# Kernel optimization log

Hardware: AMD Instinct MI355X
Metric: run time of the kernel (lower is better)

The kernel has to match this reference:

```python
import jax, jax.numpy as jnp
import numpy as np

E, T, H, I = 32, 512, 2048, 768


def setup_inputs() -> dict:
    key = jax.random.key(0)
    k1, k2, k3, k4 = jax.random.split(key, 4)
    scale = 1.0 / np.sqrt(H)
    return {
        "routed_input": jax.random.normal(k1, (E, T, H), dtype=jnp.float32),
        "gate_proj": jax.random.normal(k2, (E, I, H), dtype=jnp.float32) * scale,
        "up_proj": jax.random.normal(k3, (E, I, H), dtype=jnp.float32) * scale,
        "down_proj": jax.random.normal(k4, (E, H, I), dtype=jnp.float32) * scale,
    }


def reference(routed_input, gate_proj, up_proj, down_proj):
    # routed_input: [E, T, H]; per-expert SwiGLU MLP, concat over experts.
    gate = jnp.einsum("eth,eih->eti", routed_input, gate_proj)
    up = jnp.einsum("eth,eih->eti", routed_input, up_proj)
    hidden = jax.nn.silu(gate) * up  # [E, T, I]
    out = jnp.einsum("eti,ehi->eth", hidden, down_proj)  # [E, T, H]
    return out.reshape(E * T, H)
```

## Files before the change

kernel.cpp:

```cpp
#include <hip/hip_runtime.h>


#define NE 32
#define NT 512
#define NH 2048
#define NI 768

typedef short        short8  __attribute__((ext_vector_type(8)));
typedef float        floatx4 __attribute__((ext_vector_type(4)));
typedef unsigned int uintx4  __attribute__((ext_vector_type(4)));
typedef __attribute__((address_space(1))) const unsigned int g_u32;
typedef __attribute__((address_space(3))) unsigned int l_u32;

__device__ __forceinline__ void gl_lds16(const void* g, void* l) {
    __builtin_amdgcn_global_load_lds((g_u32*)g, (l_u32*)l, 16, 0, 0);
}

__device__ __forceinline__ unsigned int cvt_pk_bf16(float lo, float hi) {
    unsigned int r;
    asm("v_cvt_pk_bf16_f32 %0, %1, %2" : "=v"(r) : "v"(lo), "v"(hi));
    return r;
}

__device__ __forceinline__ short8 frag8(floatx4 x0, floatx4 x1) {
    union { unsigned int u[4]; short8 s; } t;
    t.u[0] = cvt_pk_bf16(x0[0], x0[1]);
    t.u[1] = cvt_pk_bf16(x0[2], x0[3]);
    t.u[2] = cvt_pk_bf16(x1[0], x1[1]);
    t.u[3] = cvt_pk_bf16(x1[2], x1[3]);
    return t.s;
}

__device__ __forceinline__ uintx4 pack8(floatx4 x0, floatx4 x1) {
    uintx4 u;
    u[0] = cvt_pk_bf16(x0[0], x0[1]);
    u[1] = cvt_pk_bf16(x0[2], x0[3]);
    u[2] = cvt_pk_bf16(x1[0], x1[1]);
    u[3] = cvt_pk_bf16(x1[2], x1[3]);
    return u;
}

__device__ __forceinline__ ushort f2bf(float f) {
    union { float f; unsigned int u; } v; v.f = f;
    unsigned int r = v.u + 0x7fffu + ((v.u >> 16) & 1u);
    return (ushort)(r >> 16);
}

__global__ __launch_bounds__(512, 1) void moe_gateup(
    const float* __restrict__ rin, const float* __restrict__ gate,
    const float* __restrict__ up, ushort* __restrict__ hidden)
{
    __shared__ ushort S[2][3][128][32];

    const int bid = blockIdx.x;
    const int wg  = (bid & 7) * 96 + (bid >> 3);
    const int e   = wg / 24;
    const int rem = wg % 24;
    const int ti  = rem % 6;
    const int tm  = rem / 6;

    const int tid  = threadIdx.x;
    const int lane = tid & 63;
    const int wave = tid >> 6;
    const int wr = wave >> 2;
    const int wc = wave & 3;

    const float* Ab = rin  + (size_t)e * NT * NH + (size_t)(tm * 128) * NH;
    const float* Gb = gate + (size_t)e * NI * NH + (size_t)(ti * 128) * NH;
    const float* Ub = up   + (size_t)e * NI * NH + (size_t)(ti * 128) * NH;

    const int s_row = wave * 16 + (lane >> 2);
    const int s_cl  = lane & 3;
    const int s_c   = s_cl ^ (s_row & 3);
    const float* As_src = Ab + (size_t)s_row * NH + s_c * 8;
    const float* Gs_src = Gb + (size_t)s_row * NH + s_c * 8;
    const float* Us_src = Ub + (size_t)s_row * NH + s_c * 8;

    floatx4 accg[4][2], accu[4][2];
    #pragma unroll
    for (int m = 0; m < 4; ++m)
        #pragma unroll
        for (int n = 0; n < 2; ++n) {
            accg[m][n] = (floatx4)0.f;
            accu[m][n] = (floatx4)0.f;
        }

    const int frow = lane & 15;
    const int h    = lane >> 4;
    const int KT = NH / 32;

    floatx4 pA0[3][2], pA1[3][2];

#define ISSUE(kt, P) do {                                                    \
        const int k_ = (kt) * 32;                                            \
        P[0][0] = *(const floatx4*)(As_src + k_);                            \
        P[0][1] = *(const floatx4*)(As_src + k_ + 4);                        \
        P[1][0] = *(const floatx4*)(Gs_src + k_);                            \
        P[1][1] = *(const floatx4*)(Gs_src + k_ + 4);                        \
        P[2][0] = *(const floatx4*)(Us_src + k_);                            \
        P[2][1] = *(const floatx4*)(Us_src + k_ + 4);                        \
    } while (0)

#define WRITE(b, P) do {                                                     \
        *(uintx4*)&S[b][0][s_row][s_cl * 8] = pack8(P[0][0], P[0][1]);       \
        *(uintx4*)&S[b][1][s_row][s_cl * 8] = pack8(P[1][0], P[1][1]);       \
        *(uintx4*)&S[b][2][s_row][s_cl * 8] = pack8(P[2][0], P[2][1]);       \
    } while (0)

#define COMPUTE(b) do {                                                      \
        short8 af[4], gf[2], uf[2];                                          \
        _Pragma("unroll")                                                    \
        for (int m = 0; m < 4; ++m) {                                        \
            const int R = wr * 64 + m * 16 + frow;                           \
            const int p = h ^ (R & 3);                                       \
            af[m] = *(const short8*)&S[b][0][R][p * 8];                      \
        }                                                                    \
        _Pragma("unroll")                                                    \
        for (int n = 0; n < 2; ++n) {                                        \
            const int R = wc * 32 + n * 16 + frow;                           \
            const int p = h ^ (R & 3);                                       \
            gf[n] = *(const short8*)&S[b][1][R][p * 8];                      \
            uf[n] = *(const short8*)&S[b][2][R][p * 8];                      \
        }                                                                    \
        _Pragma("unroll")                                                    \
        for (int m = 0; m < 4; ++m)                                          \
            _Pragma("unroll")                                                \
            for (int n = 0; n < 2; ++n) {                                    \
                accg[m][n] = __builtin_amdgcn_mfma_f32_16x16x32_bf16(        \
                    af[m], gf[n], accg[m][n], 0, 0, 0);                      \
                accu[m][n] = __builtin_amdgcn_mfma_f32_16x16x32_bf16(        \
                    af[m], uf[n], accu[m][n], 0, 0, 0);                      \
            }                                                                \
    } while (0)

#define ENDBAR() do {                                                        \
        asm volatile("s_waitcnt lgkmcnt(0)" ::: "memory");                   \
        __builtin_amdgcn_sched_barrier(0);                                   \
        __builtin_amdgcn_s_barrier();                                        \
    } while (0)

    ISSUE(0, pA0);
    ISSUE(1, pA1);
    WRITE(0, pA0);
    ENDBAR();

    for (int kt = 0; kt < KT; kt += 2) {
        if (kt + 2 < KT) ISSUE(kt + 2, pA0);
        WRITE(1, pA1);
        COMPUTE(0);
        ENDBAR();
        if (kt + 3 < KT) ISSUE(kt + 3, pA1);
        if (kt + 2 < KT) WRITE(0, pA0);
        COMPUTE(1);
        ENDBAR();
    }
#undef ISSUE
#undef WRITE
#undef COMPUTE
#undef ENDBAR

    const int ccol  = lane & 15;
    const int crow0 = (lane >> 4) * 4;
    const size_t hbase = ((size_t)e * NT + (size_t)tm * 128) * NI + ti * 128;
    #pragma unroll
    for (int m = 0; m < 4; ++m)
        #pragma unroll
        for (int n = 0; n < 2; ++n)
            #pragma unroll
            for (int j = 0; j < 4; ++j) {
                const float g = accg[m][n][j];
                const float u = accu[m][n][j];
                const float hh = (g / (1.f + __expf(-g))) * u;
                const int row = wr * 64 + m * 16 + crow0 + j;
                const int col = wc * 32 + n * 16 + ccol;
                hidden[hbase + (size_t)row * NI + col] = f2bf(hh);
            }
}

__global__ __launch_bounds__(256, 2) void moe_down(
    const ushort* __restrict__ hidden, const float* __restrict__ down,
    float* __restrict__ out)
{
    __shared__ ushort As[2][128][32];
    __shared__ float  Bs[2][128][32];

    const int bid = blockIdx.x;
    const int wg  = (bid & 7) * (2048 / 8) + (bid >> 3);
    const int e   = wg >> 6;
    const int rem = wg & 63;
    const int tn  = rem & 15;
    const int tm  = rem >> 4;

    const int tid  = threadIdx.x;
    const int lane = tid & 63;
    const int wave = tid >> 6;
    const int wr = wave >> 1, wc = wave & 1;

    const ushort* Ab = hidden + ((size_t)e * NT + (size_t)tm * 128) * NI;
    const float*  Bb = down + (size_t)e * NH * NI + (size_t)(tn * 128) * NI;

    floatx4 acc[4][4];
    #pragma unroll
    for (int m = 0; m < 4; ++m)
        #pragma unroll
        for (int n = 0; n < 4; ++n) acc[m][n] = (floatx4)0.f;

    const int frow = lane & 15;
    const int h    = lane >> 4;
    const int ca   = h ^ (frow & 3);
    const int rb   = frow & 7;
    const int c0   = (2 * h) ^ rb;
    const int c1   = (2 * h + 1) ^ rb;
    const int KT = NI / 32;

#define STAGE_DN(kt, b) do {                                                 \
        const int k0_ = (kt) * 32;                                           \
        _Pragma("unroll")                                                    \
        for (int i = 0; i < 2; ++i) {                                        \
            const int g_ = wave * 2 + i;                                     \
            const int r_ = g_ * 16 + (lane >> 2);                            \
            const int cs_ = (lane & 3) ^ (r_ & 3);                           \
            gl_lds16(Ab + (size_t)r_ * NI + k0_ + cs_ * 8, &As[b][g_ * 16][0]); \
        }                                                                    \
        _Pragma("unroll")                                                    \
        for (int i = 0; i < 4; ++i) {                                        \
            const int g_ = wave * 4 + i;                                     \
            const int r_ = g_ * 8 + (lane >> 3);                             \
            const int cs_ = (lane & 7) ^ (r_ & 7);                           \
            gl_lds16(Bb + (size_t)r_ * NI + k0_ + cs_ * 4, &Bs[b][g_ * 8][0]); \
        }                                                                    \
    } while (0)

    STAGE_DN(0, 0);

    for (int kt = 0; kt < KT; ++kt) {
        const int cur = kt & 1;
        if (kt + 1 < KT) {
            STAGE_DN(kt + 1, cur ^ 1);
            asm volatile("s_waitcnt vmcnt(6)" ::: "memory");
        } else {
            asm volatile("s_waitcnt vmcnt(0)" ::: "memory");
        }
        __builtin_amdgcn_s_barrier();

        short8 af[4], bf[4];
        #pragma unroll
        for (int m = 0; m < 4; ++m) {
            const int R = wr * 64 + m * 16 + frow;
            af[m] = *(const short8*)&As[cur][R][ca * 8];
        }
        #pragma unroll
        for (int n = 0; n < 4; ++n) {
            const int R = wc * 64 + n * 16 + frow;
            bf[n] = frag8(*(const floatx4*)&Bs[cur][R][c0 * 4],
                          *(const floatx4*)&Bs[cur][R][c1 * 4]);
        }
        #pragma unroll
        for (int m = 0; m < 4; ++m)
            #pragma unroll
            for (int n = 0; n < 4; ++n)
                acc[m][n] = __builtin_amdgcn_mfma_f32_16x16x32_bf16(
                    af[m], bf[n], acc[m][n], 0, 0, 0);

        asm volatile("s_waitcnt lgkmcnt(0)" ::: "memory");
        __builtin_amdgcn_sched_barrier(0);
        __builtin_amdgcn_s_barrier();
    }
#undef STAGE_DN

    const int ccol  = lane & 15;
    const int crow0 = (lane >> 4) * 4;
    float* Ob = out + ((size_t)e * NT + (size_t)tm * 128) * NH + tn * 128;
    #pragma unroll
    for (int m = 0; m < 4; ++m)
        #pragma unroll
        for (int n = 0; n < 4; ++n)
            #pragma unroll
            for (int j = 0; j < 4; ++j) {
                const int row = wr * 64 + m * 16 + crow0 + j;
                const int col = wc * 64 + n * 16 + ccol;
                Ob[(size_t)row * NH + col] = acc[m][n][j];
            }
}

extern "C" void kernel_launch(void* const* d_in, const int* in_sizes, int n_in,
                              void* d_out, int out_size, void* d_ws, size_t ws_size,
                              hipStream_t stream) {
    const float* rin  = (const float*)d_in[0];
    const float* gate = (const float*)d_in[1];
    const float* up   = (const float*)d_in[2];
    const float* down = (const float*)d_in[3];
    float* out = (float*)d_out;
    ushort* hidden = (ushort*)d_ws;

    moe_gateup<<<dim3(768), dim3(512), 0, stream>>>(rin, gate, up, hidden);
    moe_down<<<dim3(2048), dim3(256), 0, stream>>>(hidden, down, out);
}
```

Measured before the change: 349.6 us.

## Shrink gate/up tile to 128x64 with 256 threads and three blocks per CU

```diff
diff --git a/kernel.cpp b/kernel.cpp
--- a/kernel.cpp
+++ b/kernel.cpp
@@ -46,35 +46,42 @@
     return (ushort)(r >> 16);
 }
 
-__global__ __launch_bounds__(512, 1) void moe_gateup(
+__global__ __launch_bounds__(256, 3) void moe_gateup(
     const float* __restrict__ rin, const float* __restrict__ gate,
     const float* __restrict__ up, ushort* __restrict__ hidden)
 {
-    __shared__ ushort S[2][3][128][32];
+    __shared__ ushort SA[2][128][32];
+    __shared__ ushort SG[2][64][32];
+    __shared__ ushort SU[2][64][32];
 
     const int bid = blockIdx.x;
-    const int wg  = (bid & 7) * 96 + (bid >> 3);
-    const int e   = wg / 24;
-    const int rem = wg % 24;
-    const int ti  = rem % 6;
-    const int tm  = rem / 6;
+    const int wg  = (bid & 7) * 192 + (bid >> 3);
+    const int e   = wg / 48;
+    const int rem = wg % 48;
+    const int ti  = rem % 12;
+    const int tm  = rem / 12;
 
     const int tid  = threadIdx.x;
     const int lane = tid & 63;
     const int wave = tid >> 6;
-    const int wr = wave >> 2;
-    const int wc = wave & 3;
+    const int wr = wave >> 1;
+    const int wc = wave & 1;
 
     const float* Ab = rin  + (size_t)e * NT * NH + (size_t)(tm * 128) * NH;
-    const float* Gb = gate + (size_t)e * NI * NH + (size_t)(ti * 128) * NH;
-    const float* Ub = up   + (size_t)e * NI * NH + (size_t)(ti * 128) * NH;
-
-    const int s_row = wave * 16 + (lane >> 2);
-    const int s_cl  = lane & 3;
-    const int s_c   = s_cl ^ (s_row & 3);
-    const float* As_src = Ab + (size_t)s_row * NH + s_c * 8;
-    const float* Gs_src = Gb + (size_t)s_row * NH + s_c * 8;
-    const float* Us_src = Ub + (size_t)s_row * NH + s_c * 8;
+    const float* Gb = gate + (size_t)e * NI * NH + (size_t)(ti * 64) * NH;
+    const float* Ub = up   + (size_t)e * NI * NH + (size_t)(ti * 64) * NH;
+
+    const int a0_row = tid >> 2,            a0_cl = tid & 3;
+    const int a1_row = (tid + 256) >> 2,    a1_cl = tid & 3;
+    const int a0_c = a0_cl ^ (a0_row & 3);
+    const int a1_c = a1_cl ^ (a1_row & 3);
+    const int w_row = tid >> 2,             w_cl = tid & 3;
+    const int w_c = w_cl ^ (w_row & 3);
+
+    const float* A0src = Ab + (size_t)a0_row * NH + a0_c * 8;
+    const float* A1src = Ab + (size_t)a1_row * NH + a1_c * 8;
+    const float* Gsrc  = Gb + (size_t)w_row * NH + w_c * 8;
+    const float* Usrc  = Ub + (size_t)w_row * NH + w_c * 8;
 
     floatx4 accg[4][2], accu[4][2];
     #pragma unroll
@@ -89,22 +96,25 @@
     const int h    = lane >> 4;
     const int KT = NH / 32;
 
-    floatx4 pA0[3][2], pA1[3][2];
-
-#define ISSUE(kt, P) do {                                                    \
+    floatx4 P[4][2];
+
+#define ISSUE(kt) do {                                                       \
         const int k_ = (kt) * 32;                                            \
-        P[0][0] = *(const floatx4*)(As_src + k_);                            \
-        P[0][1] = *(const floatx4*)(As_src + k_ + 4);                        \
-        P[1][0] = *(const floatx4*)(Gs_src + k_);                            \
-        P[1][1] = *(const floatx4*)(Gs_src + k_ + 4);                        \
-        P[2][0] = *(const floatx4*)(Us_src + k_);                            \
-        P[2][1] = *(const floatx4*)(Us_src + k_ + 4);                        \
-    } while (0)
-
-#define WRITE(b, P) do {                                                     \
-        *(uintx4*)&S[b][0][s_row][s_cl * 8] = pack8(P[0][0], P[0][1]);       \
-        *(uintx4*)&S[b][1][s_row][s_cl * 8] = pack8(P[1][0], P[1][1]);       \
-        *(uintx4*)&S[b][2][s_row][s_cl * 8] = pack8(P[2][0], P[2][1]);       \
+        P[0][0] = *(const floatx4*)(A0src + k_);                             \
+        P[0][1] = *(const floatx4*)(A0src + k_ + 4);                         \
+        P[1][0] = *(const floatx4*)(A1src + k_);                             \
+        P[1][1] = *(const floatx4*)(A1src + k_ + 4);                         \
+        P[2][0] = *(const floatx4*)(Gsrc + k_);                              \
+        P[2][1] = *(const floatx4*)(Gsrc + k_ + 4);                          \
+        P[3][0] = *(const floatx4*)(Usrc + k_);                              \
+        P[3][1] = *(const floatx4*)(Usrc + k_ + 4);                          \
+    } while (0)
+
+#define WRITE(b) do {                                                       \
+        *(uintx4*)&SA[b][a0_row][a0_cl * 8] = pack8(P[0][0], P[0][1]);       \
+        *(uintx4*)&SA[b][a1_row][a1_cl * 8] = pack8(P[1][0], P[1][1]);       \
+        *(uintx4*)&SG[b][w_row][w_cl * 8]   = pack8(P[2][0], P[2][1]);       \
+        *(uintx4*)&SU[b][w_row][w_cl * 8]   = pack8(P[3][0], P[3][1]);       \
     } while (0)
 
 #define COMPUTE(b) do {                                                      \
@@ -113,14 +123,14 @@
         for (int m = 0; m < 4; ++m) {                                        \
             const int R = wr * 64 + m * 16 + frow;                           \
             const int p = h ^ (R & 3);                                       \
-            af[m] = *(const short8*)&S[b][0][R][p * 8];                      \
+            af[m] = *(const short8*)&SA[b][R][p * 8];                        \
         }                                                                    \
         _Pragma("unroll")                                                    \
         for (int n = 0; n < 2; ++n) {                                        \
             const int R = wc * 32 + n * 16 + frow;                           \
             const int p = h ^ (R & 3);                                       \
-            gf[n] = *(const short8*)&S[b][1][R][p * 8];                      \
-            uf[n] = *(const short8*)&S[b][2][R][p * 8];                      \
+            gf[n] = *(const short8*)&SG[b][R][p * 8];                        \
+            uf[n] = *(const short8*)&SU[b][R][p * 8];                        \
         }                                                                    \
         _Pragma("unroll")                                                    \
         for (int m = 0; m < 4; ++m)                                          \
@@ -139,19 +149,19 @@
         __builtin_amdgcn_s_barrier();                                        \
     } while (0)
 
-    ISSUE(0, pA0);
-    ISSUE(1, pA1);
-    WRITE(0, pA0);
+    ISSUE(0);
+    WRITE(0);
+    ISSUE(1);
     ENDBAR();
 
     for (int kt = 0; kt < KT; kt += 2) {
-        if (kt + 2 < KT) ISSUE(kt + 2, pA0);
-        WRITE(1, pA1);
         COMPUTE(0);
+        WRITE(1);
+        if (kt + 2 < KT) ISSUE(kt + 2);
         ENDBAR();
-        if (kt + 3 < KT) ISSUE(kt + 3, pA1);
-        if (kt + 2 < KT) WRITE(0, pA0);
         COMPUTE(1);
+        if (kt + 2 < KT) WRITE(0);
+        if (kt + 3 < KT) ISSUE(kt + 3);
         ENDBAR();
     }
 #undef ISSUE
@@ -161,7 +171,7 @@
 
     const int ccol  = lane & 15;
     const int crow0 = (lane >> 4) * 4;
-    const size_t hbase = ((size_t)e * NT + (size_t)tm * 128) * NI + ti * 128;
+    const size_t hbase = ((size_t)e * NT + (size_t)tm * 128) * NI + ti * 64;
     #pragma unroll
     for (int m = 0; m < 4; ++m)
         #pragma unroll
@@ -293,6 +303,6 @@
     float* out = (float*)d_out;
     ushort* hidden = (ushort*)d_ws;
 
-    moe_gateup<<<dim3(768), dim3(512), 0, stream>>>(rin, gate, up, hidden);
+    moe_gateup<<<dim3(1536), dim3(256), 0, stream>>>(rin, gate, up, hidden);
     moe_down<<<dim3(2048), dim3(256), 0, stream>>>(hidden, down, out);
 }
```

After: 336.5 us, median of 3. 1.04x faster.
